# Kernel tuning notes

Measured on AMD Instinct MI355X. Metric: run time of the kernel, lower is better.

## Reference

```python
import jax, jax.numpy as jnp
import numpy as np


def _l2norm(x, axis):
    return x / jnp.maximum(jnp.linalg.norm(x, axis=axis, keepdims=True), 1e-12)


def setup_inputs() -> dict:
    key = jax.random.key(0)
    ks = jax.random.split(key, 16)
    N, D, F, TI, HD = 1000, 100, 100, 512, 128
    # binary doc-word membership masks, ~50 words per document
    masks = (jax.random.uniform(ks[0], (D, N)) < 0.05).astype(jnp.float32)
    # sparse symmetric normalized word-graph adjacency
    a = (jax.random.uniform(ks[1], (N, N)) < 0.01).astype(jnp.float32)
    adj = jnp.maximum(a, a.T) + jnp.eye(N, dtype=jnp.float32)
    dinv = 1.0 / jnp.sqrt(adj.sum(axis=1))
    train_adj = adj * dinv[:, None] * dinv[None, :]
    bows_vec = jax.random.normal(ks[2], (N, F), dtype=jnp.float32) * 0.1
    image_features = jax.random.normal(ks[3], (D, TI), dtype=jnp.float32)

    def sc(i, sh):
        return jax.random.normal(ks[i], sh, dtype=jnp.float32) * np.float32(1.0 / np.sqrt(sh[0]))

    return {
        'epoch': 3, 'epochs': 10,
        'train_adj': train_adj, 'masks': masks, 'bows_vec': bows_vec,
        'image_features': image_features,
        'W_g1': sc(4, (F, F)), 'W_g2': sc(5, (F, F)),
        'W_h1': sc(6, (F, F)), 'b_h1': jnp.zeros(F, jnp.float32),
        'W_h2': sc(7, (F, F)), 'b_h2': jnp.zeros(F, jnp.float32),
        'W_mu2': sc(8, (F, 1)), 'b_mu2': jnp.zeros(1, jnp.float32),
        'W_eta2': sc(9, (F, 1)), 'b_eta2': jnp.zeros(1, jnp.float32),
        'W_gamma2': sc(10, (F, 1)), 'b_gamma2': jnp.zeros(1, jnp.float32),
        'w_m': sc(11, (F, 1)), 'W_beta': sc(12, (F, 1)),
        'W_m1': sc(13, (TI, HD)), 'b_m1': jnp.zeros(HD, jnp.float32),
        'W_m2': sc(14, (HD, 1)), 'b_m2': jnp.zeros(1, jnp.float32),
    }


def reference(epoch, epochs, train_adj, masks, bows_vec, image_features,
              W_g1, W_g2, W_h1, b_h1, W_h2, b_h2,
              W_mu2, b_mu2, W_eta2, b_eta2, W_gamma2, b_gamma2,
              w_m, W_beta, W_m1, b_m1, W_m2, b_m2):
    N = train_adj.shape[0]
    # --- GcnNet: 2-layer GCN over word graph; doc embedding = masked mean pool ---
    H1 = jax.nn.relu(train_adj @ (bows_vec @ W_g1))        # [N,100]
    H = train_adj @ (H1 @ W_g2)                            # [N,100]
    cnt = masks.sum(axis=1, keepdims=True)                 # [D,1]
    H_p = (masks @ H) / jnp.maximum(cnt, 1.0)              # [D,100]

    H_eli = jax.nn.relu(jax.nn.relu(H @ W_h1 + b_h1) @ W_h2 + b_h2)
    H_eli_norm = _l2norm(H_eli, axis=1)                    # [N,100]

    mu = jax.nn.relu(H_p @ W_mu2 + b_mu2)                  # [D,1]
    # dropout disabled (eval mode)
    eta = jax.nn.relu(H_p @ W_eta2 + b_eta2)               # [D,1]
    gamma = jax.nn.relu(H_p @ W_gamma2 + b_gamma2)         # [D,1]

    sparsity = (epoch / epochs) * 0.3                      # python float (static)
    flat = w_m.reshape(-1)
    j = int(round(sparsity * flat.shape[0]))
    order = jnp.argsort(flat)                              # ascending; drop lowest j
    binary = jnp.zeros_like(flat).at[order[j:]].set(1.0)
    mask_ste = flat + jax.lax.stop_gradient(binary - flat) # forward==binary
    w_pruned = mask_ste.reshape(-1, 1) * W_beta            # [100,1]
    beta_ = _l2norm((H @ w_pruned)[:, 0], axis=0)          # [N]
    beta = masks @ beta_[:, None]                          # [D,1]

    Z_ = jax.nn.relu(H_eli_norm @ H_eli_norm.T)            # [N,N]

    # per-doc sum over distinct word pairs of h_i . h_j ; ||h||=1 so
    # sum_{a<b} h_a.h_b = (||sum_a h_a||^2 - k)/2 with k = #words in doc
    s = masks @ H_eli_norm                                 # [D,100]
    k = masks.sum(axis=1)                                  # [D]
    Z = jax.nn.relu(0.5 * (jnp.sum(s * s, axis=1) - k))[:, None]  # [D,1]

    # Z_event: per-doc [N,N] with entries at local positions p,q < k_i (p!=q)
    # (original indexes Z_ with LOCAL sorted positions 0..k_i-1; kept faithful)
    pos = jnp.arange(N)
    valid = (pos[None, :] < k[:, None]).astype(jnp.float32)       # [D,N]
    E = jnp.exp(-jnp.square(2.0 - 2.0 * Z_)) * (1.0 - jnp.eye(N)) # [N,N]
    Z_event = E[None, :, :] * valid[:, :, None] * valid[:, None, :]  # [D,N,N]

    lambda_texts = jax.nn.sigmoid(mu + beta + eta * jnp.exp(-gamma * Z))
    h_img = jax.nn.relu(image_features @ W_m1 + b_m1)
    lambda_imgs = h_img @ W_m2 + b_m2                      # MLP(512,128,1)
    lambda_total = jax.nn.sigmoid(lambda_texts + lambda_imgs)
    return (lambda_total, Z_, beta_, gamma, eta, Z_event, H)
```

## Files before the change

kernel.cpp:

```cpp
#include <hip/hip_runtime.h>
#include <hip/hip_bf16.h>

typedef __hip_bfloat16 bf;

#define NN   1000
#define DD   100
#define FF   100
#define TIF  512
#define HDD  128
#define EB   256
#define ACAP 96
#define MCAP 192

#define O_LAM 0
#define O_Z   100
#define O_B3  1000100
#define O_GAM 1001100
#define O_ETA 1001200
#define O_ZE  1001300
#define O_H   101001300

__device__ __forceinline__ float ldf(const void* p, int i, int F32){
  return F32 ? ((const float*)p)[i] : __bfloat162float(((const __hip_bfloat16*)p)[i]);
}

__device__ __forceinline__ float blk_red(float v, volatile float* red, int tid){
#pragma unroll
  for (int o=32;o>0;o>>=1) v += __shfl_down(v,o,64);
  if ((tid&63)==0) red[tid>>6]=v;
  __syncthreads();
  float r = red[0]+red[1];
  __syncthreads();
  return r;
}
__device__ __forceinline__ float blk_red4(float v, volatile float* red, int tid){
#pragma unroll
  for (int o=32;o>0;o>>=1) v += __shfl_down(v,o,64);
  if ((tid&63)==0) red[tid>>6]=v;
  __syncthreads();
  float r = red[0]+red[1]+red[2]+red[3];
  __syncthreads();
  return r;
}

__device__ __forceinline__ int sniffF32(const unsigned short* __restrict__ p, int tid){
  int lane = tid & 63;
  const ushort4* q = (const ushort4*)p;
  ushort4 a = q[lane*2], b = q[lane*2+1];
  int c = 0;
  c += (((a.x>>7)&0xFF)>=0xE0); c += (((a.y>>7)&0xFF)>=0xE0);
  c += (((a.z>>7)&0xFF)>=0xE0); c += (((a.w>>7)&0xFF)>=0xE0);
  c += (((b.x>>7)&0xFF)>=0xE0); c += (((b.y>>7)&0xFF)>=0xE0);
  c += (((b.z>>7)&0xFF)>=0xE0); c += (((b.w>>7)&0xFF)>=0xE0);
#pragma unroll
  for (int o=32;o>0;o>>=1) c += __shfl_xor(c,o,64);
  return c > 8;
}

__device__ __forceinline__ void zero_span(uint4* __restrict__ zb, long off, long cnt,
                                          int zi, int nzb, int tid, int bdim){
  long per = (cnt + nzb - 1)/nzb;
  long s = (long)zi*per; if (s>cnt) s=cnt;
  long e = s+per; if (e>cnt) e=cnt;
  uint4 z; z.x=z.y=z.z=z.w=0u;
  for (long i=off+s+tid; i<off+e; i+=bdim) zb[i]=z;
}

__global__ void k1_build(const void* __restrict__ A, const void* __restrict__ masks,
                         const void* __restrict__ wm, const void* __restrict__ Wbeta,
                         const void* __restrict__ img, const void* __restrict__ Wm1,
                         const void* __restrict__ bm1, const void* __restrict__ Wm2,
                         const void* __restrict__ bm2, const void* __restrict__ X,
                         const void* __restrict__ Wg1,
                         const int* epoch, const int* epochs,
                         int* a_idx, float* a_val, int* a_nnz,
                         int* m_idx, int* m_cnt, float* wpr, float* sumsq,
                         float* limg, int* flag, float* __restrict__ XW,
                         uint4* __restrict__ zb){
  int b = blockIdx.x; int lane = threadIdx.x;
  if (b >= NN+DD+1+DD+NN){ zero_span(zb, 0L, 8000000L, b-(NN+DD+1+DD+NN), 2048, lane, 64); return; }
  int F32 = sniffF32((const unsigned short*)X, lane);
  if (b < NN){
    int i=b, nn=0;
    for (int base=0;base<NN;base+=64){
      int c=base+lane; float v=0.f;
      if (c<NN) v=ldf(A, i*NN+c, F32);
      unsigned long long m=__ballot(v!=0.f);
      if (v!=0.f){
        int pos=nn+__popcll(m&((1ull<<lane)-1ull));
        if (pos<ACAP){ a_idx[i*ACAP+pos]=c; a_val[i*ACAP+pos]=v; }
      }
      nn+=__popcll(m);
    }
    if (lane==0) a_nnz[i]=min(nn,ACAP);
  } else if (b < NN+DD){
    int d=b-NN, nn=0;
    for (int base=0;base<NN;base+=64){
      int c=base+lane; float v=0.f;
      if (c<NN) v=ldf(masks, d*NN+c, F32);
      unsigned long long m=__ballot(v!=0.f);
      if (v!=0.f){
        int pos=nn+__popcll(m&((1ull<<lane)-1ull));
        if (pos<MCAP) m_idx[d*MCAP+pos]=c;
      }
      nn+=__popcll(m);
    }
    if (lane==0) m_cnt[d]=min(nn,MCAP);
  } else if (b == NN+DD){
    __shared__ float w[FF];
    for (int t=lane;t<FF;t+=64) w[t]=ldf(wm, t, F32);
    __syncthreads();
    float sp = 0.3f*(float)epoch[0]/(float)epochs[0];
    int j=(int)lroundf(sp*(float)FF);
    for (int t=lane;t<FF;t+=64){
      float v=w[t]; int r=0;
      for (int u=0;u<FF;u++){ float vu=w[u]; r += ((vu<v)||(vu==v && u<t)) ? 1 : 0; }
      wpr[t] = (r>=j)? ldf(Wbeta, t, F32) : 0.f;
    }
    if (lane==0){ sumsq[0]=0.f; flag[0]=F32; }
  } else if (b < NN+DD+1+DD){
    int d = b - (NN+DD+1);
    __shared__ float ir[TIF];
    for (int t=lane;t<TIF;t+=64) ir[t]=ldf(img, d*TIF+t, F32);
    __syncthreads();
    float acc=0.f;
    for (int h=lane; h<HDD; h+=64){
      float a=ldf(bm1, h, F32);
#pragma unroll 4
      for (int t=0;t<TIF;t++) a=fmaf(ir[t], ldf(Wm1, t*HDD+h, F32), a);
      acc = fmaf(fmaxf(a,0.f), ldf(Wm2, h, F32), acc);
    }
#pragma unroll
    for (int o=32;o>0;o>>=1) acc += __shfl_down(acc,o,64);
    if (lane==0) limg[d]=acc+ldf(bm2,0,F32);
  } else {
    int r = b - (NN+DD+1+DD);
    __shared__ float ar[FF];
    for (int t=lane;t<FF;t+=64) ar[t]=ldf(X, r*FF+t, F32);
    __syncthreads();
    for (int col=lane; col<FF; col+=64){
      float a=0.f;
#pragma unroll 4
      for (int c=0;c<FF;c++) a=fmaf(ar[c], ldf(Wg1, c*FF+col, F32), a);
      XW[r*FF+col]=a;
    }
  }
}

__global__ void k2_h1(const float* __restrict__ XW, const void* __restrict__ Wg2,
                      const int* flag, const int* __restrict__ a_idx,
                      const float* __restrict__ a_val, const int* __restrict__ a_nnz,
                      float* __restrict__ H1W, uint4* __restrict__ zb){
  int row=blockIdx.x, tx=threadIdx.x;
  if (row >= NN){ zero_span(zb, 8000000L, 5000000L, row-NN, 1280, tx, 128); return; }
  __shared__ int sidx[ACAP]; __shared__ float sval[ACAP]; __shared__ float t1[FF];
  int nn=a_nnz[row];
  for (int t=tx;t<nn;t+=128){ sidx[t]=a_idx[row*ACAP+t]; sval[t]=a_val[row*ACAP+t]; }
  __syncthreads();
  if (tx<FF){
    float a=0.f;
    for (int m=0;m<nn;m++) a=fmaf(sval[m], XW[sidx[m]*FF+tx], a);
    t1[tx]=fmaxf(a,0.f);
  }
  __syncthreads();
  int F32=flag[0];
  if (tx<FF){
    float s=0.f;
#pragma unroll 4
    for (int c=0;c<FF;c++) s=fmaf(t1[c], ldf(Wg2, c*FF+tx, F32), s);
    H1W[row*FF+tx]=s;
  }
}

__global__ void k3_h2(const float* __restrict__ H1W, const int* __restrict__ a_idx,
                      const float* __restrict__ a_val, const int* __restrict__ a_nnz,
                      const void* __restrict__ Wh1, const void* __restrict__ bh1,
                      const void* __restrict__ Wh2, const void* __restrict__ bh2,
                      const float* __restrict__ wpr, const int* flag,
                      float* __restrict__ Hh, float* __restrict__ Hn,
                      float* __restrict__ HnT, float* __restrict__ hw, float* sumsq,
                      float* __restrict__ outH, uint4* __restrict__ zb){
  int i=blockIdx.x, tx=threadIdx.x;
  if (i >= NN){ zero_span(zb, 13000000L, 5000000L, i-NN, 1280, tx, 128); return; }
  __shared__ int sidx[ACAP]; __shared__ float sval[ACAP];
  __shared__ float hr[FF], t1[FF];
  __shared__ float red[2];
  int nn=a_nnz[i];
  for (int t=tx;t<nn;t+=128){ sidx[t]=a_idx[i*ACAP+t]; sval[t]=a_val[i*ACAP+t]; }
  __syncthreads();
  if (tx<FF){
    float a=0.f;
    for (int m=0;m<nn;m++) a=fmaf(sval[m], H1W[sidx[m]*FF+tx], a);
    hr[tx]=a; Hh[i*FF+tx]=a; outH[i*FF+tx]=a;
  }
  __syncthreads();
  int F32=flag[0];
  if (tx<FF){
    float a=ldf(bh1, tx, F32);
#pragma unroll 4
    for (int c=0;c<FF;c++) a=fmaf(hr[c], ldf(Wh1, c*FF+tx, F32), a);
    t1[tx]=fmaxf(a,0.f);
  }
  __syncthreads();
  float hel=0.f;
  if (tx<FF){
    float s=ldf(bh2, tx, F32);
#pragma unroll 4
    for (int c=0;c<FF;c++) s=fmaf(t1[c], ldf(Wh2, c*FF+tx, F32), s);
    hel=fmaxf(s,0.f);
  }
  float phw = (tx<FF)? hr[tx]*wpr[tx] : 0.f;
  float rs2 = blk_red(hel*hel, red, tx);
  float rhw = blk_red(phw, red, tx);
  float rinv = 1.f/fmaxf(sqrtf(rs2), 1e-12f);
  if (tx<FF){ float v=hel*rinv; Hn[i*FF+tx]=v; HnT[tx*NN+i]=v; }
  if (tx==0){ hw[i]=rhw; atomicAdd(sumsq, rhw*rhw); }
}

__global__ __launch_bounds__(256) void k4_zdoc(const float* __restrict__ HnT,
                      const float* __restrict__ Hh, const float* __restrict__ Hn,
                      const float* __restrict__ hw, const float* __restrict__ sumsq,
                      const int* __restrict__ m_idx, const int* __restrict__ m_cnt,
                      const void* Wmu, const void* bmu, const void* Weta, const void* beta_b,
                      const void* Wgam, const void* bgam, const int* flag,
                      const float* __restrict__ limg,
                      float* __restrict__ out, float* __restrict__ Eblk,
                      uint4* __restrict__ zb){
  int b=blockIdx.x, tid=threadIdx.x;
  if (b >= 360){ zero_span(zb, 18000000L, 7000000L, b-360, 1792, tid, 256); return; }
  if (b < 256){
    int bi=(b&15)*64, bj=(b>>4)*64;
    __shared__ float At[FF*68], Bt[FF*68];
    for (int t=tid;t<FF*64;t+=256){
      int k=t>>6, ii=t&63;
      int gi=bi+ii, gj=bj+ii;
      At[k*68+ii] = (gi<NN)? HnT[k*NN+gi] : 0.f;
      Bt[k*68+ii] = (gj<NN)? HnT[k*NN+gj] : 0.f;
    }
    __syncthreads();
    int tx=tid&15, ty=tid>>4;
    float acc[4][4]={};
    for (int k=0;k<FF;k++){
      float4 av=*(float4*)&At[k*68+4*ty];
      float4 bv=*(float4*)&Bt[k*68+4*tx];
      float aa[4]={av.x,av.y,av.z,av.w};
      float bb[4]={bv.x,bv.y,bv.z,bv.w};
#pragma unroll
      for (int q=0;q<4;q++)
#pragma unroll
        for (int r=0;r<4;r++) acc[q][r]=fmaf(aa[q],bb[r],acc[q][r]);
    }
#pragma unroll
    for (int q=0;q<4;q++){
      int gi=bi+4*ty+q; if (gi>=NN) continue;
      float z[4];
#pragma unroll
      for (int r=0;r<4;r++) z[r]=fmaxf(acc[q][r],0.f);
      int gj0=bj+4*tx;
      if (gj0+3<NN){
        float4 zz; zz.x=z[0]; zz.y=z[1]; zz.z=z[2]; zz.w=z[3];
        *(float4*)&out[O_Z+(size_t)gi*NN+gj0]=zz;
      } else {
        for (int r=0;r<4;r++) if (gj0+r<NN) out[O_Z+(size_t)gi*NN+gj0+r]=z[r];
      }
      if (gi<EB && gj0<EB){
#pragma unroll
        for (int r=0;r<4;r++){
          int gj=gj0+r;
          float t2=2.f-2.f*z[r];
          Eblk[gi*EB+gj]=(gi==gj)?0.f:expf(-t2*t2);
        }
      }
    }
    return;
  }
  if (b >= 356){
    int i=(b-356)*256+tid;
    if (i<NN){
      float rinv=1.f/fmaxf(sqrtf(sumsq[0]),1e-12f);
      out[O_B3+i]=hw[i]*rinv;
    }
    return;
  }
  int d=b-256;
  int F32 = flag[0];
  __shared__ int sidx[MCAP]; __shared__ float red[4];
  int cnt=m_cnt[d];
  for (int t=tid;t<cnt;t+=256) sidx[t]=m_idx[d*MCAP+t];
  __syncthreads();
  float accH=0.f, accS=0.f;
  if (tid<FF) for (int m=0;m<cnt;m++){ int n=sidx[m]; accH+=Hh[n*FF+tid]; accS+=Hn[n*FF+tid]; }
  float Hp = accH/fmaxf((float)cnt,1.f);
  float pmu = (tid<FF)? Hp*ldf(Wmu, tid, F32)  : 0.f;
  float peta= (tid<FF)? Hp*ldf(Weta, tid, F32) : 0.f;
  float pgam= (tid<FF)? Hp*ldf(Wgam, tid, F32) : 0.f;
  float phw=0.f;
  for (int m=tid;m<cnt;m+=256) phw+=hw[sidx[m]];
  float rmu =blk_red4(pmu,red,tid);
  float reta=blk_red4(peta,red,tid);
  float rgam=blk_red4(pgam,red,tid);
  float rs2 =blk_red4(accS*accS,red,tid);
  float rhw =blk_red4(phw,red,tid);
  if (tid==0){
    float mu =fmaxf(rmu +ldf(bmu,0,F32),   0.f);
    float eta=fmaxf(reta+ldf(beta_b,0,F32),0.f);
    float gam=fmaxf(rgam+ldf(bgam,0,F32),  0.f);
    float Zd =fmaxf(0.5f*(rs2-(float)cnt), 0.f);
    float beta=rhw/fmaxf(sqrtf(sumsq[0]),1e-12f);
    float lt=1.f/(1.f+expf(-(mu+beta+eta*expf(-gam*Zd))));
    out[O_LAM+d]=1.f/(1.f+expf(-(lt+limg[d])));
    out[O_GAM+d]=gam;
    out[O_ETA+d]=eta;
  }
}

__global__ void k5_fill(const float* __restrict__ Eblk, const int* __restrict__ m_cnt,
                        float* __restrict__ outZE){
  int d=blockIdx.x; int k=m_cnt[d]; if (k>EB) k=EB;
  int kk=k*k;
  for (int idx=threadIdx.x; idx<kk; idx+=256){
    int i=idx/k, j=idx-i*k;
    float e=(i==j)?0.f:Eblk[i*EB+j];
    outZE[(size_t)d*1000000 + (size_t)i*1000 + j]=e;
  }
}

extern "C" void kernel_launch(void* const* d_in, const int* in_sizes, int n_in,
                              void* d_out, int out_size, void* d_ws, size_t ws_size,
                              hipStream_t stream) {
  const int* epoch  = (const int*)d_in[0];
  const int* epochs = (const int*)d_in[1];
  const void* A     = d_in[2];
  const void* masks = d_in[3];
  const void* X     = d_in[4];
  const void* img   = d_in[5];
  const void* Wg1   = d_in[6];
  const void* Wg2   = d_in[7];
  const void* Wh1   = d_in[8];
  const void* bh1   = d_in[9];
  const void* Wh2   = d_in[10];
  const void* bh2   = d_in[11];
  const void* Wmu   = d_in[12];
  const void* bmu   = d_in[13];
  const void* Weta  = d_in[14];
  const void* beta_b= d_in[15];
  const void* Wgam  = d_in[16];
  const void* bgam  = d_in[17];
  const void* wm    = d_in[18];
  const void* Wbeta = d_in[19];
  const void* Wm1   = d_in[20];
  const void* bm1   = d_in[21];
  const void* Wm2   = d_in[22];
  const void* bm2   = d_in[23];
  float* out = (float*)d_out;

  float* ws   = (float*)d_ws;
  float* XW   = ws;
  float* H1W  = XW  + 100000;
  float* Hh   = H1W + 100000;
  float* Hn   = Hh  + 100000;
  float* HnT  = Hn  + 100000;
  float* Eblk = HnT + 100000;
  float* a_val= Eblk+ 65536;
  int* a_idx  = (int*)(a_val + 96000);
  int* a_nnz  = a_idx + 96000;
  int* m_idx  = a_nnz + 1000;
  int* m_cnt  = m_idx + 19200;
  float* wpr  = (float*)(m_cnt + 100);
  float* hw   = wpr + 100;
  float* sumsq= hw + 1000;
  int* flag   = (int*)(sumsq + 4);
  float* limg = (float*)(flag + 4);

  uint4* zb = (uint4*)((char*)d_out + (size_t)O_ZE*4);

  hipLaunchKernelGGL(k1_build, dim3(NN+DD+1+DD+NN+2048), dim3(64), 0, stream,
                     A, masks, wm, Wbeta, img, Wm1, bm1, Wm2, bm2, X, Wg1,
                     epoch, epochs,
                     a_idx, a_val, a_nnz, m_idx, m_cnt, wpr, sumsq, limg, flag, XW, zb);
  hipLaunchKernelGGL(k2_h1, dim3(NN+1280), dim3(128), 0, stream,
                     XW, Wg2, flag, a_idx, a_val, a_nnz, H1W, zb);
  hipLaunchKernelGGL(k3_h2, dim3(NN+1280), dim3(128), 0, stream,
                     H1W, a_idx, a_val, a_nnz, Wh1, bh1, Wh2, bh2, wpr, flag,
                     Hh, Hn, HnT, hw, sumsq, out + O_H, zb);
  hipLaunchKernelGGL(k4_zdoc, dim3(360+1792), dim3(256), 0, stream,
                     HnT, Hh, Hn, hw, sumsq, m_idx, m_cnt,
                     Wmu, bmu, Weta, beta_b, Wgam, bgam, flag, limg,
                     out, Eblk, zb);
  hipLaunchKernelGGL(k5_fill, dim3(DD), dim3(256), 0, stream, Eblk, m_cnt, out + O_ZE);
}
```

Baseline: 668.7 us.

## Fuse Z_event fill into doc kernel and split zeroing into prefix/tail regions

```diff
diff --git a/kernel.cpp b/kernel.cpp
--- a/kernel.cpp
+++ b/kernel.cpp
@@ -2,15 +2,16 @@
 #include <hip/hip_bf16.h>
 
 typedef __hip_bfloat16 bf;
+typedef unsigned int u32x4 __attribute__((ext_vector_type(4)));
 
 #define NN   1000
 #define DD   100
 #define FF   100
 #define TIF  512
 #define HDD  128
-#define EB   256
 #define ACAP 96
 #define MCAP 192
+#define KCAP 96
 
 #define O_LAM 0
 #define O_Z   100
@@ -19,6 +20,12 @@
 #define O_ETA 1001200
 #define O_ZE  1001300
 #define O_H   101001300
+
+#define SLABU4 250000u
+#define PREFU4 32000u
+#define TAILU4 218000u
+#define NPREF  3200000u
+#define NTAIL  21800000u
 
 __device__ __forceinline__ float ldf(const void* p, int i, int F32){
   return F32 ? ((const float*)p)[i] : __bfloat162float(((const __hip_bfloat16*)p)[i]);
@@ -57,13 +64,30 @@
   return c > 8;
 }
 
-__device__ __forceinline__ void zero_span(uint4* __restrict__ zb, long off, long cnt,
+__device__ __forceinline__ void zero_pref(u32x4* __restrict__ zb, int zi, int nzb,
+                                          int tid, int bdim){
+  unsigned per = (NPREF + nzb - 1)/nzb;
+  unsigned s = min((unsigned)zi*per, NPREF);
+  unsigned e = min(s+per, NPREF);
+  u32x4 z = (u32x4)(0u);
+  for (unsigned t=s+tid; t<e; t+=bdim){
+    unsigned slab = t / PREFU4;
+    unsigned off  = t - slab*PREFU4;
+    zb[(long)slab*SLABU4 + off] = z;
+  }
+}
+__device__ __forceinline__ void zero_tail(u32x4* __restrict__ zb, unsigned t0, unsigned t1,
                                           int zi, int nzb, int tid, int bdim){
-  long per = (cnt + nzb - 1)/nzb;
-  long s = (long)zi*per; if (s>cnt) s=cnt;
-  long e = s+per; if (e>cnt) e=cnt;
-  uint4 z; z.x=z.y=z.z=z.w=0u;
-  for (long i=off+s+tid; i<off+e; i+=bdim) zb[i]=z;
+  unsigned cnt = t1-t0;
+  unsigned per = (cnt + nzb - 1)/nzb;
+  unsigned s = t0 + min((unsigned)zi*per, cnt);
+  unsigned e = t0 + min((unsigned)zi*per+per, cnt);
+  u32x4 z = (u32x4)(0u);
+  for (unsigned t=s+tid; t<e; t+=bdim){
+    unsigned slab = t / TAILU4;
+    unsigned off  = t - slab*TAILU4 + PREFU4;
+    zb[(long)slab*SLABU4 + off] = z;
+  }
 }
 
 __global__ void k1_build(const void* __restrict__ A, const void* __restrict__ masks,
@@ -76,9 +100,15 @@
                          int* a_idx, float* a_val, int* a_nnz,
                          int* m_idx, int* m_cnt, float* wpr, float* sumsq,
                          float* limg, int* flag, float* __restrict__ XW,
-                         uint4* __restrict__ zb){
+                         u32x4* __restrict__ zb){
   int b = blockIdx.x; int lane = threadIdx.x;
-  if (b >= NN+DD+1+DD+NN){ zero_span(zb, 0L, 8000000L, b-(NN+DD+1+DD+NN), 2048, lane, 64); return; }
+  const int NB = NN+DD+1+DD+NN;
+  if (b >= NB){
+    int zi = b - NB;
+    if (zi < 1024) zero_pref(zb, zi, 1024, lane, 64);
+    else           zero_tail(zb, 0u, 2800000u, zi-1024, 1024, lane, 64);
+    return;
+  }
   int F32 = sniffF32((const unsigned short*)X, lane);
   if (b < NN){
     int i=b, nn=0;
@@ -150,9 +180,9 @@
 __global__ void k2_h1(const float* __restrict__ XW, const void* __restrict__ Wg2,
                       const int* flag, const int* __restrict__ a_idx,
                       const float* __restrict__ a_val, const int* __restrict__ a_nnz,
-                      float* __restrict__ H1W, uint4* __restrict__ zb){
+                      float* __restrict__ H1W, u32x4* __restrict__ zb){
   int row=blockIdx.x, tx=threadIdx.x;
-  if (row >= NN){ zero_span(zb, 8000000L, 5000000L, row-NN, 1280, tx, 128); return; }
+  if (row >= NN){ zero_tail(zb, 2800000u, 8800000u, row-NN, 1280, tx, 128); return; }
   __shared__ int sidx[ACAP]; __shared__ float sval[ACAP]; __shared__ float t1[FF];
   int nn=a_nnz[row];
   for (int t=tx;t<nn;t+=128){ sidx[t]=a_idx[row*ACAP+t]; sval[t]=a_val[row*ACAP+t]; }
@@ -179,9 +209,9 @@
                       const float* __restrict__ wpr, const int* flag,
                       float* __restrict__ Hh, float* __restrict__ Hn,
                       float* __restrict__ HnT, float* __restrict__ hw, float* sumsq,
-                      float* __restrict__ outH, uint4* __restrict__ zb){
+                      float* __restrict__ outH, u32x4* __restrict__ zb){
   int i=blockIdx.x, tx=threadIdx.x;
-  if (i >= NN){ zero_span(zb, 13000000L, 5000000L, i-NN, 1280, tx, 128); return; }
+  if (i >= NN){ zero_tail(zb, 8800000u, 14800000u, i-NN, 1280, tx, 128); return; }
   __shared__ int sidx[ACAP]; __shared__ float sval[ACAP];
   __shared__ float hr[FF], t1[FF];
   __shared__ float red[2];
@@ -224,25 +254,28 @@
                       const void* Wmu, const void* bmu, const void* Weta, const void* beta_b,
                       const void* Wgam, const void* bgam, const int* flag,
                       const float* __restrict__ limg,
-                      float* __restrict__ out, float* __restrict__ Eblk,
-                      uint4* __restrict__ zb){
+                      float* __restrict__ out, u32x4* __restrict__ zb){
   int b=blockIdx.x, tid=threadIdx.x;
-  if (b >= 360){ zero_span(zb, 18000000L, 7000000L, b-360, 1792, tid, 256); return; }
+  if (b >= 360){ zero_tail(zb, 14800000u, 21800000u, b-360, 1792, tid, 256); return; }
+  __shared__ union U {
+    struct { float At[FF*68]; float Bt[FF*68]; } zt;
+    struct { float hn[KCAP*FF]; } doc;
+    __device__ U(){}
+  } sh;
   if (b < 256){
     int bi=(b&15)*64, bj=(b>>4)*64;
-    __shared__ float At[FF*68], Bt[FF*68];
     for (int t=tid;t<FF*64;t+=256){
       int k=t>>6, ii=t&63;
       int gi=bi+ii, gj=bj+ii;
-      At[k*68+ii] = (gi<NN)? HnT[k*NN+gi] : 0.f;
-      Bt[k*68+ii] = (gj<NN)? HnT[k*NN+gj] : 0.f;
+      sh.zt.At[k*68+ii] = (gi<NN)? HnT[k*NN+gi] : 0.f;
+      sh.zt.Bt[k*68+ii] = (gj<NN)? HnT[k*NN+gj] : 0.f;
     }
     __syncthreads();
     int tx=tid&15, ty=tid>>4;
     float acc[4][4]={};
     for (int k=0;k<FF;k++){
-      float4 av=*(float4*)&At[k*68+4*ty];
-      float4 bv=*(float4*)&Bt[k*68+4*tx];
+      float4 av=*(float4*)&sh.zt.At[k*68+4*ty];
+      float4 bv=*(float4*)&sh.zt.Bt[k*68+4*tx];
       float aa[4]={av.x,av.y,av.z,av.w};
       float bb[4]={bv.x,bv.y,bv.z,bv.w};
 #pragma unroll
@@ -262,14 +295,6 @@
         *(float4*)&out[O_Z+(size_t)gi*NN+gj0]=zz;
       } else {
         for (int r=0;r<4;r++) if (gj0+r<NN) out[O_Z+(size_t)gi*NN+gj0+r]=z[r];
-      }
-      if (gi<EB && gj0<EB){
-#pragma unroll
-        for (int r=0;r<4;r++){
-          int gj=gj0+r;
-          float t2=2.f-2.f*z[r];
-          Eblk[gi*EB+gj]=(gi==gj)?0.f:expf(-t2*t2);
-        }
       }
     }
     return;
@@ -312,16 +337,27 @@
     out[O_GAM+d]=gam;
     out[O_ETA+d]=eta;
   }
-}
-
-__global__ void k5_fill(const float* __restrict__ Eblk, const int* __restrict__ m_cnt,
-                        float* __restrict__ outZE){
-  int d=blockIdx.x; int k=m_cnt[d]; if (k>EB) k=EB;
-  int kk=k*k;
-  for (int idx=threadIdx.x; idx<kk; idx+=256){
+  int k = min(cnt, KCAP);
+  for (int t=tid; t<k*FF; t+=256) sh.doc.hn[t]=Hn[t];
+  __syncthreads();
+  float* outZE = out + O_ZE + (size_t)d*1000000;
+  for (int idx=tid; idx<k*k; idx+=256){
     int i=idx/k, j=idx-i*k;
-    float e=(i==j)?0.f:Eblk[i*EB+j];
-    outZE[(size_t)d*1000000 + (size_t)i*1000 + j]=e;
+    float v=0.f;
+    if (i!=j){
+      const float4* hi=(const float4*)&sh.doc.hn[i*FF];
+      const float4* hj=(const float4*)&sh.doc.hn[j*FF];
+      float a=0.f;
+#pragma unroll
+      for (int c=0;c<25;c++){
+        float4 x=hi[c], y=hj[c];
+        a=fmaf(x.x,y.x,a); a=fmaf(x.y,y.y,a); a=fmaf(x.z,y.z,a); a=fmaf(x.w,y.w,a);
+      }
+      a=fmaxf(a,0.f);
+      float t2=2.f-2.f*a;
+      v=expf(-t2*t2);
+    }
+    outZE[(size_t)i*1000 + j]=v;
   }
 }
 
@@ -360,8 +396,7 @@
   float* Hh   = H1W + 100000;
   float* Hn   = Hh  + 100000;
   float* HnT  = Hn  + 100000;
-  float* Eblk = HnT + 100000;
-  float* a_val= Eblk+ 65536;
+  float* a_val= HnT + 100000;
   int* a_idx  = (int*)(a_val + 96000);
   int* a_nnz  = a_idx + 96000;
   int* m_idx  = a_nnz + 1000;
@@ -372,7 +407,7 @@
   int* flag   = (int*)(sumsq + 4);
   float* limg = (float*)(flag + 4);
 
-  uint4* zb = (uint4*)((char*)d_out + (size_t)O_ZE*4);
+  u32x4* zb = (u32x4*)((char*)d_out + (size_t)O_ZE*4);
 
   hipLaunchKernelGGL(k1_build, dim3(NN+DD+1+DD+NN+2048), dim3(64), 0, stream,
                      A, masks, wm, Wbeta, img, Wm1, bm1, Wm2, bm2, X, Wg1,
@@ -386,6 +421,5 @@
   hipLaunchKernelGGL(k4_zdoc, dim3(360+1792), dim3(256), 0, stream,
                      HnT, Hh, Hn, hw, sumsq, m_idx, m_cnt,
                      Wmu, bmu, Weta, beta_b, Wgam, bgam, flag, limg,
-                     out, Eblk, zb);
-  hipLaunchKernelGGL(k5_fill, dim3(DD), dim3(256), 0, stream, Eblk, m_cnt, out + O_ZE);
-}
+                     out, zb);
+}
```

After: 670.5 us. Within noise of the previous version (+0.3%).
